# Performance work log

Hardware: AMD Instinct MI355X
Metric: run time of the kernel (lower is better)

## Reference

```python
import jax, jax.numpy as jnp
import numpy as np
import math

N = 512
XDIM = 256
EDIM = 128
N_HEAD = 8
DF = XDIM // N_HEAD


def _linear(x, W, b):
    # torch nn.Linear: y = x @ W.T + b, W is [out, in]
    return x @ W.T + b


def setup_inputs() -> dict:
    key = jax.random.key(0)
    ks = jax.random.split(key, 20)
    s = 0.02
    inp = {
        "x": jax.random.normal(ks[0], (N, XDIM), jnp.float32),
        "e": jax.random.normal(ks[1], (N, N, EDIM), jnp.float32),
        "adj": jax.random.uniform(ks[2], (N, N), jnp.float32),
        "Wq": jax.random.normal(ks[3], (XDIM, XDIM), jnp.float32) * s,
        "bq": jnp.zeros((XDIM,), jnp.float32),
        "Wk": jax.random.normal(ks[4], (XDIM, XDIM), jnp.float32) * s,
        "bk": jnp.zeros((XDIM,), jnp.float32),
        "Wv": jax.random.normal(ks[5], (XDIM, XDIM), jnp.float32) * s,
        "bv": jnp.zeros((XDIM,), jnp.float32),
        "Wem": jax.random.normal(ks[6], (XDIM, EDIM), jnp.float32) * s,
        "bem": jnp.zeros((XDIM,), jnp.float32),
        "Wea": jax.random.normal(ks[7], (XDIM, EDIM), jnp.float32) * s,
        "bea": jnp.zeros((XDIM,), jnp.float32),
        "Wxo": jax.random.normal(ks[8], (XDIM, XDIM), jnp.float32) * s,
        "bxo": jnp.zeros((XDIM,), jnp.float32),
        "Weo": jax.random.normal(ks[9], (EDIM, XDIM), jnp.float32) * s,
        "beo": jnp.zeros((EDIM,), jnp.float32),
    }
    return inp


def reference(x, e, adj, Wq, bq, Wk, bk, Wv, bv, Wem, bem, Wea, bea, Wxo, bxo, Weo, beo):
    n = x.shape[0]
    Q = _linear(x, Wq, bq).reshape(n, N_HEAD, DF)  # [N, H, df]
    K = _linear(x, Wk, bk).reshape(n, N_HEAD, DF)
    # elementwise (non-dot) score: [N, N, H, df]
    Y = (Q[:, None, :, :] * K[None, :, :, :]) / math.sqrt(DF)
    E1 = _linear(e, Wem, bem).reshape(n, n, N_HEAD, DF)
    E2 = _linear(e, Wea, bea).reshape(n, n, N_HEAD, DF)
    Y = Y * (E1 + 1.0) + E2
    newE = _linear(Y.reshape(n, n, XDIM), Weo, beo)  # [N, N, edim]
    attn = jax.nn.softmax(Y, axis=1)  # softmax over key-node axis (dim=1)
    V = _linear(x, Wv, bv).reshape(n, N_HEAD, DF)
    weighted_V = (attn * V[None, :, :, :]).sum(axis=1)  # [N, H, df]
    newX = _linear(weighted_V.reshape(n, XDIM), Wxo, bxo)
    return (newX, newE)
```

## Files before the change

### kernel.cpp

```cpp
#include <hip/hip_runtime.h>
#include <math.h>

#define NN 512
#define XD 256
#define ED 128
#define JC 32
#define NCHUNK (NN/JC)

typedef __attribute__((ext_vector_type(8))) short s8v;
typedef __attribute__((ext_vector_type(4))) float f4v;

__device__ __forceinline__ short f2bf(float f) {
    union { float f; unsigned u; } v; v.f = f;
    unsigned r = (v.u + 0x7FFFu + ((v.u >> 16) & 1u)) >> 16;
    return (short)r;
}
__device__ __forceinline__ s8v load8_bf(const float* __restrict__ p) {
    const float4* p4 = (const float4*)p;
    float4 a = p4[0], b = p4[1];
    s8v r;
    r[0]=f2bf(a.x); r[1]=f2bf(a.y); r[2]=f2bf(a.z); r[3]=f2bf(a.w);
    r[4]=f2bf(b.x); r[5]=f2bf(b.y); r[6]=f2bf(b.z); r[7]=f2bf(b.w);
    return r;
}
__device__ __forceinline__ float bf2f(short s) {
    union { unsigned u; float f; } v;
    v.u = ((unsigned)(unsigned short)s) << 16;
    return v.f;
}

__global__ void wconv_kernel(const float* __restrict__ Wem, const float* __restrict__ Wea,
                             const float* __restrict__ Weo,
                             short* __restrict__ Wem_bf, short* __restrict__ Wea_bf,
                             short* __restrict__ Weo_bf) {
    const int f = blockIdx.x * 256 + threadIdx.x;
    const int lane = f & 63;
    const int quad = lane >> 4;
    const int l16  = lane & 15;
    if (blockIdx.y < 2) {
        const float* src = blockIdx.y == 0 ? Wem : Wea;
        short* dst = blockIdx.y == 0 ? Wem_bf : Wea_bf;
        const int cb = f >> 8;
        const int ks = (f >> 6) & 3;
        *(s8v*)(dst + (size_t)f * 8) =
            load8_bf(src + (size_t)(cb*16 + l16)*ED + ks*32 + quad*8);
    } else {
        const int ob = f >> 9;
        const int ks = (f >> 6) & 7;
        *(s8v*)(Weo_bf + (size_t)f * 8) =
            load8_bf(Weo + (size_t)(ob*16 + l16)*XD + ks*32 + quad*8);
    }
}

__global__ void qkv_kernel(const float* __restrict__ x,
                           const float* __restrict__ Wq, const float* __restrict__ bq,
                           const float* __restrict__ Wk, const float* __restrict__ bk,
                           const float* __restrict__ Wv, const float* __restrict__ bv,
                           float* __restrict__ out) {
    const int i = blockIdx.x, which = blockIdx.y, t = threadIdx.x;
    __shared__ float sx[XD];
    sx[t] = x[i*XD + t];
    __syncthreads();
    const float* W = which==0 ? Wq : (which==1 ? Wk : Wv);
    const float* b = which==0 ? bq : (which==1 ? bk : bv);
    const float4* W4 = (const float4*)(W + (size_t)t*XD);
    const float4* x4 = (const float4*)sx;
    float acc = 0.f;
    #pragma unroll 8
    for (int k4 = 0; k4 < XD/4; ++k4) {
        float4 w = W4[k4]; float4 xv = x4[k4];
        acc += w.x*xv.x + w.y*xv.y + w.z*xv.z + w.w*xv.w;
    }
    acc += b[t];
    if (which == 0) acc *= 0.17677669529663688f;
    out[((size_t)which*NN + i)*XD + t] = acc;
}

#define SE_STRIDE 136
#define SY_STRIDE 264

__global__ __launch_bounds__(512, 4) void pass1_kernel(
    const float* __restrict__ e,
    const float* __restrict__ Qs, const float* __restrict__ Km, const float* __restrict__ Vm,
    const short* __restrict__ Wem_bf, const float* __restrict__ bem,
    const short* __restrict__ Wea_bf, const float* __restrict__ bea,
    const short* __restrict__ Weo_bf, const float* __restrict__ beo,
    float* __restrict__ outE,
    float* __restrict__ Pm, float* __restrict__ Pl, float* __restrict__ Pa)
{
    __shared__ short sE[JC*SE_STRIDE];
    __shared__ short sY[JC*SY_STRIDE];

    const int ch = blockIdx.x;
    const int i  = blockIdx.y;
    const int t = threadIdx.x;
    const int wave = t >> 6;
    const int lane = t & 63;
    const int quad = (lane >> 4) & 3;
    const int l16 = lane & 15;

    const int wn0 = wave * 32;
    float q_l[2], bm1[2], bea_l[2];
    #pragma unroll
    for (int nt = 0; nt < 2; ++nt) {
        const int c = wn0 + nt*16 + l16;
        q_l[nt]   = Qs[i*XD + c];
        bm1[nt]   = bem[c] + 1.0f;
        bea_l[nt] = bea[c];
    }
    const int oo = wave*16 + l16;
    const float beo_l = beo[oo];

    const s8v* W1p = (const s8v*)(Wem_bf + ((size_t)wave*8*64 + lane)*8);
    const s8v* W2p = (const s8v*)(Wea_bf + ((size_t)wave*8*64 + lane)*8);
    const s8v* W3p = (const s8v*)(Weo_bf + ((size_t)wave*8*64 + lane)*8);

    {
        const int j  = t >> 4;
        const int k0 = (t & 15) * 8;
        const float* src = e + ((size_t)i*NN + (size_t)(ch*JC + j))*ED + k0;
        *(s8v*)(&sE[j*SE_STRIDE + k0]) = load8_bf(src);
    }
    __syncthreads();

    f4v acc1[2][2], acc2[2][2];
    #pragma unroll
    for (int mt = 0; mt < 2; ++mt)
        #pragma unroll
        for (int nt = 0; nt < 2; ++nt) {
            f4v z = {0.f, 0.f, 0.f, 0.f};
            acc1[mt][nt] = z; acc2[mt][nt] = z;
        }
    #pragma unroll
    for (int ks = 0; ks < 4; ++ks) {
        s8v a0 = *(const s8v*)(&sE[(     l16)*SE_STRIDE + ks*32 + quad*8]);
        s8v a1 = *(const s8v*)(&sE[(16 + l16)*SE_STRIDE + ks*32 + quad*8]);
        #pragma unroll
        for (int nt = 0; nt < 2; ++nt) {
            s8v b1 = W1p[(nt*4 + ks)*64];
            s8v b2 = W2p[(nt*4 + ks)*64];
            acc1[0][nt] = __builtin_amdgcn_mfma_f32_16x16x32_bf16(a0, b1, acc1[0][nt], 0, 0, 0);
            acc1[1][nt] = __builtin_amdgcn_mfma_f32_16x16x32_bf16(a1, b1, acc1[1][nt], 0, 0, 0);
            acc2[0][nt] = __builtin_amdgcn_mfma_f32_16x16x32_bf16(a0, b2, acc2[0][nt], 0, 0, 0);
            acc2[1][nt] = __builtin_amdgcn_mfma_f32_16x16x32_bf16(a1, b2, acc2[1][nt], 0, 0, 0);
        }
    }

    #pragma unroll
    for (int mt = 0; mt < 2; ++mt) {
        const int jlb = mt*16 + quad*4;
        const int jgb = ch*JC + jlb;
        #pragma unroll
        for (int nt = 0; nt < 2; ++nt) {
            const int c = wn0 + nt*16 + l16;
            #pragma unroll
            for (int r = 0; r < 4; ++r) {
                float e1 = acc1[mt][nt][r] + bm1[nt];
                float e2 = acc2[mt][nt][r] + bea_l[nt];
                float kv = Km[(size_t)(jgb + r)*XD + c];
                float y  = q_l[nt]*kv*e1 + e2;
                sY[(jlb + r)*SY_STRIDE + c] = f2bf(y);
            }
        }
    }
    __syncthreads();

    f4v acc3[2];
    {
        f4v z = {0.f, 0.f, 0.f, 0.f};
        acc3[0] = z; acc3[1] = z;
    }
    #pragma unroll
    for (int ks = 0; ks < 8; ++ks) {
        s8v b3 = W3p[ks*64];
        s8v a0 = *(const s8v*)(&sY[(     l16)*SY_STRIDE + ks*32 + quad*8]);
        s8v a1 = *(const s8v*)(&sY[(16 + l16)*SY_STRIDE + ks*32 + quad*8]);
        acc3[0] = __builtin_amdgcn_mfma_f32_16x16x32_bf16(a0, b3, acc3[0], 0, 0, 0);
        acc3[1] = __builtin_amdgcn_mfma_f32_16x16x32_bf16(a1, b3, acc3[1], 0, 0, 0);
    }
    #pragma unroll
    for (int mt = 0; mt < 2; ++mt) {
        const int jlb = mt*16 + quad*4;
        #pragma unroll
        for (int r = 0; r < 4; ++r) {
            const int jg = ch*JC + jlb + r;
            outE[((size_t)i*NN + jg)*ED + oo] = acc3[mt][r] + beo_l;
        }
    }

    const int sc_c  = t & 255;
    const int sc_jh = t >> 8;
    float m_run = -INFINITY, l_run = 0.f, a_run = 0.f;
    #pragma unroll
    for (int jj = 0; jj < 16; ++jj) {
        const int jl = sc_jh*16 + jj;
        const int jg = ch*JC + jl;
        float y  = bf2f(sY[jl*SY_STRIDE + sc_c]);
        float v  = Vm[(size_t)jg*XD + sc_c];
        float mn = fmaxf(m_run, y);
        float s0 = __expf(m_run - mn);
        float p  = __expf(y - mn);
        l_run = l_run*s0 + p;
        a_run = a_run*s0 + p*v;
        m_run = mn;
    }
    __syncthreads();
    float* sRed = (float*)sE;
    float* sRed2 = (float*)sY;
    sRed[t] = m_run; sRed2[t] = l_run; sRed2[512 + t] = a_run;
    __syncthreads();
    if (t < 256) {
        float m0 = sRed[t],       m1 = sRed[256 + t];
        float l0 = sRed2[t],      l1 = sRed2[256 + t];
        float a0 = sRed2[512+t],  a1 = sRed2[768 + t];
        float M  = fmaxf(m0, m1);
        float e0 = __expf(m0 - M), e1x = __expf(m1 - M);
        const size_t pb = ((size_t)i*NCHUNK + ch)*256 + t;
        Pm[pb] = M;
        Pl[pb] = l0*e0 + l1*e1x;
        Pa[pb] = a0*e0 + a1*e1x;
    }
}

__global__ void pass2_kernel(const float* __restrict__ Pm, const float* __restrict__ Pl,
                             const float* __restrict__ Pa,
                             const float* __restrict__ Wxo, const float* __restrict__ bxo,
                             float* __restrict__ outX) {
    const int i = blockIdx.x, t = threadIdx.x;
    float mloc[NCHUNK];
    float M = -INFINITY;
    #pragma unroll
    for (int ch = 0; ch < NCHUNK; ++ch) {
        mloc[ch] = Pm[((size_t)i*NCHUNK + ch)*256 + t];
        M = fmaxf(M, mloc[ch]);
    }
    float L = 0.f, A = 0.f;
    #pragma unroll
    for (int ch = 0; ch < NCHUNK; ++ch) {
        const size_t pb = ((size_t)i*NCHUNK + ch)*256 + t;
        float s = __expf(mloc[ch] - M);
        L += Pl[pb]*s;
        A += Pa[pb]*s;
    }
    __shared__ float sv[XD];
    sv[t] = A / L;
    __syncthreads();
    const float4* W4 = (const float4*)(Wxo + (size_t)t*XD);
    const float4* v4 = (const float4*)sv;
    float acc = 0.f;
    #pragma unroll 8
    for (int k4 = 0; k4 < XD/4; ++k4) {
        float4 w = W4[k4]; float4 v = v4[k4];
        acc += w.x*v.x + w.y*v.y + w.z*v.z + w.w*v.w;
    }
    outX[(size_t)i*XD + t] = acc + bxo[t];
}

extern "C" void kernel_launch(void* const* d_in, const int* in_sizes, int n_in,
                              void* d_out, int out_size, void* d_ws, size_t ws_size,
                              hipStream_t stream) {
    const float* x   = (const float*)d_in[0];
    const float* e   = (const float*)d_in[1];
    const float* Wq  = (const float*)d_in[3];
    const float* bq  = (const float*)d_in[4];
    const float* Wk  = (const float*)d_in[5];
    const float* bk  = (const float*)d_in[6];
    const float* Wv  = (const float*)d_in[7];
    const float* bv  = (const float*)d_in[8];
    const float* Wem = (const float*)d_in[9];
    const float* bem = (const float*)d_in[10];
    const float* Wea = (const float*)d_in[11];
    const float* bea = (const float*)d_in[12];
    const float* Wxo = (const float*)d_in[13];
    const float* bxo = (const float*)d_in[14];
    const float* Weo = (const float*)d_in[15];
    const float* beo = (const float*)d_in[16];

    float* ws = (float*)d_ws;
    float* Qs = ws;
    float* Km = ws + (size_t)NN*XD;
    float* Vm = ws + (size_t)2*NN*XD;
    float* Pm = ws + (size_t)3*NN*XD;
    float* Pl = Pm + (size_t)NN*NCHUNK*XD;
    float* Pa = Pl + (size_t)NN*NCHUNK*XD;
    short* Wem_bf = (short*)(Pa + (size_t)NN*NCHUNK*XD);
    short* Wea_bf = Wem_bf + (size_t)XD*ED;
    short* Weo_bf = Wea_bf + (size_t)XD*ED;

    float* outX = (float*)d_out;
    float* outE = outX + (size_t)NN*XD;

    wconv_kernel<<<dim3(16, 3), 256, 0, stream>>>(Wem, Wea, Weo, Wem_bf, Wea_bf, Weo_bf);
    qkv_kernel<<<dim3(NN, 3), 256, 0, stream>>>(x, Wq, bq, Wk, bk, Wv, bv, ws);
    pass1_kernel<<<dim3(NCHUNK, NN), 512, 0, stream>>>(e, Qs, Km, Vm,
                                                       Wem_bf, bem, Wea_bf, bea,
                                                       Weo_bf, beo, outE, Pm, Pl, Pa);
    pass2_kernel<<<NN, 256, 0, stream>>>(Pm, Pl, Pa, Wxo, bxo, outX);
}
```

Measured before the change: 389.9 us.

## Fuse pass1 and pass2 into one persistent-per-row kernel with double-buffered e prefetch

```diff
diff --git a/kernel.cpp b/kernel.cpp
--- a/kernel.cpp
+++ b/kernel.cpp
@@ -6,6 +6,8 @@
 #define ED 128
 #define JC 32
 #define NCHUNK (NN/JC)
+#define SE_STRIDE 136
+#define SY_STRIDE 264
 
 typedef __attribute__((ext_vector_type(8))) short s8v;
 typedef __attribute__((ext_vector_type(4))) float f4v;
@@ -23,10 +25,10 @@
     r[4]=f2bf(b.x); r[5]=f2bf(b.y); r[6]=f2bf(b.z); r[7]=f2bf(b.w);
     return r;
 }
-__device__ __forceinline__ float bf2f(short s) {
-    union { unsigned u; float f; } v;
-    v.u = ((unsigned)(unsigned short)s) << 16;
-    return v.f;
+__device__ __forceinline__ unsigned cvt_pk_bf16(float lo, float hi) {
+    unsigned r;
+    asm("v_cvt_pk_bf16_f32 %0, %1, %2" : "=v"(r) : "v"(lo), "v"(hi));
+    return r;
 }
 
 __global__ void wconv_kernel(const float* __restrict__ Wem, const float* __restrict__ Wea,
@@ -76,30 +78,26 @@
     out[((size_t)which*NN + i)*XD + t] = acc;
 }
 
-#define SE_STRIDE 136
-#define SY_STRIDE 264
-
-__global__ __launch_bounds__(512, 4) void pass1_kernel(
+__global__ __launch_bounds__(512, 4) void fused_kernel(
     const float* __restrict__ e,
     const float* __restrict__ Qs, const float* __restrict__ Km, const float* __restrict__ Vm,
     const short* __restrict__ Wem_bf, const float* __restrict__ bem,
     const short* __restrict__ Wea_bf, const float* __restrict__ bea,
     const short* __restrict__ Weo_bf, const float* __restrict__ beo,
-    float* __restrict__ outE,
-    float* __restrict__ Pm, float* __restrict__ Pl, float* __restrict__ Pa)
+    const float* __restrict__ Wxo, const float* __restrict__ bxo,
+    float* __restrict__ outX, float* __restrict__ outE)
 {
-    __shared__ short sE[JC*SE_STRIDE];
-    __shared__ short sY[JC*SY_STRIDE];
-
-    const int ch = blockIdx.x;
-    const int i  = blockIdx.y;
+    __shared__ __align__(16) short sE[2][JC*SE_STRIDE];
+    __shared__ __align__(16) short sY[JC*SY_STRIDE];
+
+    const int i = blockIdx.x;
     const int t = threadIdx.x;
     const int wave = t >> 6;
     const int lane = t & 63;
     const int quad = (lane >> 4) & 3;
-    const int l16 = lane & 15;
-
-    const int wn0 = wave * 32;
+    const int l16  = lane & 15;
+    const int wn0  = wave * 32;
+
     float q_l[2], bm1[2], bea_l[2];
     #pragma unroll
     for (int nt = 0; nt < 2; ++nt) {
@@ -115,145 +113,175 @@
     const s8v* W2p = (const s8v*)(Wea_bf + ((size_t)wave*8*64 + lane)*8);
     const s8v* W3p = (const s8v*)(Weo_bf + ((size_t)wave*8*64 + lane)*8);
 
+    const int sj = t >> 4;
+    const int sk = (t & 15) * 8;
+    const float4* esrc = (const float4*)(e + ((size_t)i*NN + sj)*ED + sk);
+
+    float rm[2] = {-INFINITY, -INFINITY};
+    float rl[2] = {0.f, 0.f};
+    float ra[2] = {0.f, 0.f};
+
+    float4 pfa = esrc[0], pfb = esrc[1];
     {
-        const int j  = t >> 4;
-        const int k0 = (t & 15) * 8;
-        const float* src = e + ((size_t)i*NN + (size_t)(ch*JC + j))*ED + k0;
-        *(s8v*)(&sE[j*SE_STRIDE + k0]) = load8_bf(src);
-    }
+        unsigned u0 = cvt_pk_bf16(pfa.x, pfa.y), u1 = cvt_pk_bf16(pfa.z, pfa.w);
+        unsigned u2 = cvt_pk_bf16(pfb.x, pfb.y), u3 = cvt_pk_bf16(pfb.z, pfb.w);
+        int4 pk; pk.x=(int)u0; pk.y=(int)u1; pk.z=(int)u2; pk.w=(int)u3;
+        *(int4*)(&sE[0][sj*SE_STRIDE + sk]) = pk;
+    }
+    int cur = 0;
+
+    #pragma unroll 1
+    for (int ch = 0; ch < NCHUNK; ++ch) {
+        const bool more = (ch + 1 < NCHUNK);
+        if (more) {
+            const float4* p = esrc + (size_t)(ch+1)*1024;
+            pfa = p[0]; pfb = p[1];
+        }
+        __syncthreads();
+
+        f4v acc1[2][2], acc2[2][2];
+        #pragma unroll
+        for (int mt = 0; mt < 2; ++mt)
+            #pragma unroll
+            for (int nt = 0; nt < 2; ++nt) {
+                f4v z = {0.f, 0.f, 0.f, 0.f};
+                acc1[mt][nt] = z; acc2[mt][nt] = z;
+            }
+        #pragma unroll
+        for (int ks = 0; ks < 4; ++ks) {
+            s8v a0 = *(const s8v*)(&sE[cur][(     l16)*SE_STRIDE + ks*32 + quad*8]);
+            s8v a1 = *(const s8v*)(&sE[cur][(16 + l16)*SE_STRIDE + ks*32 + quad*8]);
+            #pragma unroll
+            for (int nt = 0; nt < 2; ++nt) {
+                s8v b1 = W1p[(nt*4 + ks)*64];
+                s8v b2 = W2p[(nt*4 + ks)*64];
+                acc1[0][nt] = __builtin_amdgcn_mfma_f32_16x16x32_bf16(a0, b1, acc1[0][nt], 0, 0, 0);
+                acc1[1][nt] = __builtin_amdgcn_mfma_f32_16x16x32_bf16(a1, b1, acc1[1][nt], 0, 0, 0);
+                acc2[0][nt] = __builtin_amdgcn_mfma_f32_16x16x32_bf16(a0, b2, acc2[0][nt], 0, 0, 0);
+                acc2[1][nt] = __builtin_amdgcn_mfma_f32_16x16x32_bf16(a1, b2, acc2[1][nt], 0, 0, 0);
+            }
+        }
+
+        float y[2][2][4];
+        const float* Kb = Km + ((size_t)ch*JC + quad*4)*XD + wn0 + l16;
+        #pragma unroll
+        for (int mt = 0; mt < 2; ++mt)
+            #pragma unroll
+            for (int nt = 0; nt < 2; ++nt)
+                #pragma unroll
+                for (int r = 0; r < 4; ++r) {
+                    float e1 = acc1[mt][nt][r] + bm1[nt];
+                    float e2 = acc2[mt][nt][r] + bea_l[nt];
+                    float kv = Kb[(mt*16 + r)*XD + nt*16];
+                    y[mt][nt][r] = q_l[nt]*kv*e1 + e2;
+                }
+
+        #pragma unroll
+        for (int mt = 0; mt < 2; ++mt)
+            #pragma unroll
+            for (int nt = 0; nt < 2; ++nt) {
+                unsigned p01 = cvt_pk_bf16(y[mt][nt][0], y[mt][nt][1]);
+                unsigned p23 = cvt_pk_bf16(y[mt][nt][2], y[mt][nt][3]);
+                short* b = &sY[(mt*16 + quad*4)*SY_STRIDE + wn0 + nt*16 + l16];
+                b[0]            = (short)p01;
+                b[SY_STRIDE]    = (short)(p01 >> 16);
+                b[2*SY_STRIDE]  = (short)p23;
+                b[3*SY_STRIDE]  = (short)(p23 >> 16);
+            }
+
+        {
+            const float* Vb = Vm + ((size_t)ch*JC + quad*4)*XD + wn0 + l16;
+            float vv[2][2][4];
+            #pragma unroll
+            for (int mt = 0; mt < 2; ++mt)
+                #pragma unroll
+                for (int nt = 0; nt < 2; ++nt)
+                    #pragma unroll
+                    for (int r = 0; r < 4; ++r)
+                        vv[mt][nt][r] = Vb[(mt*16 + r)*XD + nt*16];
+            #pragma unroll
+            for (int nt = 0; nt < 2; ++nt) {
+                float mc = fmaxf(
+                    fmaxf(fmaxf(y[0][nt][0], y[0][nt][1]), fmaxf(y[0][nt][2], y[0][nt][3])),
+                    fmaxf(fmaxf(y[1][nt][0], y[1][nt][1]), fmaxf(y[1][nt][2], y[1][nt][3])));
+                float mn = fmaxf(rm[nt], mc);
+                float s  = __expf(rm[nt] - mn);
+                float l0 = rl[nt]*s, a0 = ra[nt]*s;
+                float l1 = 0.f,      a1 = 0.f;
+                #pragma unroll
+                for (int r = 0; r < 4; ++r) {
+                    float p0 = __expf(y[0][nt][r] - mn);
+                    float p1 = __expf(y[1][nt][r] - mn);
+                    l0 += p0; a0 += p0 * vv[0][nt][r];
+                    l1 += p1; a1 += p1 * vv[1][nt][r];
+                }
+                rl[nt] = l0 + l1; ra[nt] = a0 + a1; rm[nt] = mn;
+            }
+        }
+
+        __syncthreads();
+
+        f4v acc3[2];
+        {
+            f4v z = {0.f, 0.f, 0.f, 0.f};
+            acc3[0] = z; acc3[1] = z;
+        }
+        #pragma unroll
+        for (int ks = 0; ks < 8; ++ks) {
+            s8v b3 = W3p[ks*64];
+            s8v a0 = *(const s8v*)(&sY[(     l16)*SY_STRIDE + ks*32 + quad*8]);
+            s8v a1 = *(const s8v*)(&sY[(16 + l16)*SY_STRIDE + ks*32 + quad*8]);
+            acc3[0] = __builtin_amdgcn_mfma_f32_16x16x32_bf16(a0, b3, acc3[0], 0, 0, 0);
+            acc3[1] = __builtin_amdgcn_mfma_f32_16x16x32_bf16(a1, b3, acc3[1], 0, 0, 0);
+        }
+        #pragma unroll
+        for (int mt = 0; mt < 2; ++mt)
+            #pragma unroll
+            for (int r = 0; r < 4; ++r) {
+                const int jg = ch*JC + mt*16 + quad*4 + r;
+                outE[((size_t)i*NN + jg)*ED + oo] = acc3[mt][r] + beo_l;
+            }
+
+        if (more) {
+            unsigned u0 = cvt_pk_bf16(pfa.x, pfa.y), u1 = cvt_pk_bf16(pfa.z, pfa.w);
+            unsigned u2 = cvt_pk_bf16(pfb.x, pfb.y), u3 = cvt_pk_bf16(pfb.z, pfb.w);
+            int4 pk; pk.x=(int)u0; pk.y=(int)u1; pk.z=(int)u2; pk.w=(int)u3;
+            *(int4*)(&sE[cur ^ 1][sj*SE_STRIDE + sk]) = pk;
+            cur ^= 1;
+        }
+    }
+
     __syncthreads();
-
-    f4v acc1[2][2], acc2[2][2];
+    float* sv = (float*)sY;
     #pragma unroll
-    for (int mt = 0; mt < 2; ++mt)
-        #pragma unroll
-        for (int nt = 0; nt < 2; ++nt) {
-            f4v z = {0.f, 0.f, 0.f, 0.f};
-            acc1[mt][nt] = z; acc2[mt][nt] = z;
-        }
-    #pragma unroll
-    for (int ks = 0; ks < 4; ++ks) {
-        s8v a0 = *(const s8v*)(&sE[(     l16)*SE_STRIDE + ks*32 + quad*8]);
-        s8v a1 = *(const s8v*)(&sE[(16 + l16)*SE_STRIDE + ks*32 + quad*8]);
-        #pragma unroll
-        for (int nt = 0; nt < 2; ++nt) {
-            s8v b1 = W1p[(nt*4 + ks)*64];
-            s8v b2 = W2p[(nt*4 + ks)*64];
-            acc1[0][nt] = __builtin_amdgcn_mfma_f32_16x16x32_bf16(a0, b1, acc1[0][nt], 0, 0, 0);
-            acc1[1][nt] = __builtin_amdgcn_mfma_f32_16x16x32_bf16(a1, b1, acc1[1][nt], 0, 0, 0);
-            acc2[0][nt] = __builtin_amdgcn_mfma_f32_16x16x32_bf16(a0, b2, acc2[0][nt], 0, 0, 0);
-            acc2[1][nt] = __builtin_amdgcn_mfma_f32_16x16x32_bf16(a1, b2, acc2[1][nt], 0, 0, 0);
-        }
-    }
-
-    #pragma unroll
-    for (int mt = 0; mt < 2; ++mt) {
-        const int jlb = mt*16 + quad*4;
-        const int jgb = ch*JC + jlb;
-        #pragma unroll
-        for (int nt = 0; nt < 2; ++nt) {
-            const int c = wn0 + nt*16 + l16;
-            #pragma unroll
-            for (int r = 0; r < 4; ++r) {
-                float e1 = acc1[mt][nt][r] + bm1[nt];
-                float e2 = acc2[mt][nt][r] + bea_l[nt];
-                float kv = Km[(size_t)(jgb + r)*XD + c];
-                float y  = q_l[nt]*kv*e1 + e2;
-                sY[(jlb + r)*SY_STRIDE + c] = f2bf(y);
-            }
-        }
+    for (int nt = 0; nt < 2; ++nt) {
+        #pragma unroll
+        for (int off = 16; off < 64; off <<= 1) {
+            float mo = __shfl_xor(rm[nt], off);
+            float lo = __shfl_xor(rl[nt], off);
+            float ao = __shfl_xor(ra[nt], off);
+            float mn = fmaxf(rm[nt], mo);
+            float s  = __expf(rm[nt] - mn);
+            float so = __expf(mo - mn);
+            rl[nt] = rl[nt]*s + lo*so;
+            ra[nt] = ra[nt]*s + ao*so;
+            rm[nt] = mn;
+        }
+        if (quad == 0) sv[wn0 + nt*16 + l16] = ra[nt] / rl[nt];
     }
     __syncthreads();
 
-    f4v acc3[2];
-    {
-        f4v z = {0.f, 0.f, 0.f, 0.f};
-        acc3[0] = z; acc3[1] = z;
-    }
-    #pragma unroll
-    for (int ks = 0; ks < 8; ++ks) {
-        s8v b3 = W3p[ks*64];
-        s8v a0 = *(const s8v*)(&sY[(     l16)*SY_STRIDE + ks*32 + quad*8]);
-        s8v a1 = *(const s8v*)(&sY[(16 + l16)*SY_STRIDE + ks*32 + quad*8]);
-        acc3[0] = __builtin_amdgcn_mfma_f32_16x16x32_bf16(a0, b3, acc3[0], 0, 0, 0);
-        acc3[1] = __builtin_amdgcn_mfma_f32_16x16x32_bf16(a1, b3, acc3[1], 0, 0, 0);
-    }
-    #pragma unroll
-    for (int mt = 0; mt < 2; ++mt) {
-        const int jlb = mt*16 + quad*4;
-        #pragma unroll
-        for (int r = 0; r < 4; ++r) {
-            const int jg = ch*JC + jlb + r;
-            outE[((size_t)i*NN + jg)*ED + oo] = acc3[mt][r] + beo_l;
-        }
-    }
-
-    const int sc_c  = t & 255;
-    const int sc_jh = t >> 8;
-    float m_run = -INFINITY, l_run = 0.f, a_run = 0.f;
-    #pragma unroll
-    for (int jj = 0; jj < 16; ++jj) {
-        const int jl = sc_jh*16 + jj;
-        const int jg = ch*JC + jl;
-        float y  = bf2f(sY[jl*SY_STRIDE + sc_c]);
-        float v  = Vm[(size_t)jg*XD + sc_c];
-        float mn = fmaxf(m_run, y);
-        float s0 = __expf(m_run - mn);
-        float p  = __expf(y - mn);
-        l_run = l_run*s0 + p;
-        a_run = a_run*s0 + p*v;
-        m_run = mn;
-    }
-    __syncthreads();
-    float* sRed = (float*)sE;
-    float* sRed2 = (float*)sY;
-    sRed[t] = m_run; sRed2[t] = l_run; sRed2[512 + t] = a_run;
-    __syncthreads();
-    if (t < 256) {
-        float m0 = sRed[t],       m1 = sRed[256 + t];
-        float l0 = sRed2[t],      l1 = sRed2[256 + t];
-        float a0 = sRed2[512+t],  a1 = sRed2[768 + t];
-        float M  = fmaxf(m0, m1);
-        float e0 = __expf(m0 - M), e1x = __expf(m1 - M);
-        const size_t pb = ((size_t)i*NCHUNK + ch)*256 + t;
-        Pm[pb] = M;
-        Pl[pb] = l0*e0 + l1*e1x;
-        Pa[pb] = a0*e0 + a1*e1x;
-    }
-}
-
-__global__ void pass2_kernel(const float* __restrict__ Pm, const float* __restrict__ Pl,
-                             const float* __restrict__ Pa,
-                             const float* __restrict__ Wxo, const float* __restrict__ bxo,
-                             float* __restrict__ outX) {
-    const int i = blockIdx.x, t = threadIdx.x;
-    float mloc[NCHUNK];
-    float M = -INFINITY;
-    #pragma unroll
-    for (int ch = 0; ch < NCHUNK; ++ch) {
-        mloc[ch] = Pm[((size_t)i*NCHUNK + ch)*256 + t];
-        M = fmaxf(M, mloc[ch]);
-    }
-    float L = 0.f, A = 0.f;
-    #pragma unroll
-    for (int ch = 0; ch < NCHUNK; ++ch) {
-        const size_t pb = ((size_t)i*NCHUNK + ch)*256 + t;
-        float s = __expf(mloc[ch] - M);
-        L += Pl[pb]*s;
-        A += Pa[pb]*s;
-    }
-    __shared__ float sv[XD];
-    sv[t] = A / L;
-    __syncthreads();
-    const float4* W4 = (const float4*)(Wxo + (size_t)t*XD);
-    const float4* v4 = (const float4*)sv;
-    float acc = 0.f;
-    #pragma unroll 8
-    for (int k4 = 0; k4 < XD/4; ++k4) {
-        float4 w = W4[k4]; float4 v = v4[k4];
-        acc += w.x*v.x + w.y*v.y + w.z*v.z + w.w*v.w;
-    }
-    outX[(size_t)i*XD + t] = acc + bxo[t];
+    if (t < XD) {
+        const float4* W4 = (const float4*)(Wxo + (size_t)t*XD);
+        const float4* v4 = (const float4*)sv;
+        float acc = 0.f;
+        #pragma unroll 8
+        for (int k4 = 0; k4 < XD/4; ++k4) {
+            float4 w = W4[k4]; float4 v = v4[k4];
+            acc += w.x*v.x + w.y*v.y + w.z*v.z + w.w*v.w;
+        }
+        outX[(size_t)i*XD + t] = acc + bxo[t];
+    }
 }
 
 extern "C" void kernel_launch(void* const* d_in, const int* in_sizes, int n_in,
@@ -280,10 +308,7 @@
     float* Qs = ws;
     float* Km = ws + (size_t)NN*XD;
     float* Vm = ws + (size_t)2*NN*XD;
-    float* Pm = ws + (size_t)3*NN*XD;
-    float* Pl = Pm + (size_t)NN*NCHUNK*XD;
-    float* Pa = Pl + (size_t)NN*NCHUNK*XD;
-    short* Wem_bf = (short*)(Pa + (size_t)NN*NCHUNK*XD);
+    short* Wem_bf = (short*)(ws + (size_t)3*NN*XD);
     short* Wea_bf = Wem_bf + (size_t)XD*ED;
     short* Weo_bf = Wea_bf + (size_t)XD*ED;
 
@@ -292,8 +317,7 @@
 
     wconv_kernel<<<dim3(16, 3), 256, 0, stream>>>(Wem, Wea, Weo, Wem_bf, Wea_bf, Weo_bf);
     qkv_kernel<<<dim3(NN, 3), 256, 0, stream>>>(x, Wq, bq, Wk, bk, Wv, bv, ws);
-    pass1_kernel<<<dim3(NCHUNK, NN), 512, 0, stream>>>(e, Qs, Km, Vm,
-                                                       Wem_bf, bem, Wea_bf, bea,
-                                                       Weo_bf, beo, outE, Pm, Pl, Pa);
-    pass2_kernel<<<NN, 256, 0, stream>>>(Pm, Pl, Pa, Wxo, bxo, outX);
-}
+    fused_kernel<<<NN, 512, 0, stream>>>(e, Qs, Km, Vm,
+                                         Wem_bf, bem, Wea_bf, bea, Weo_bf, beo,
+                                         Wxo, bxo, outX, outE);
+}
```

Measured after the change: 482.8 us. 1.24x slower.

## Compute chunk softmax partials from MFMA registers with wave shuffles

Applied to the files above, without the earlier changes.

```diff
diff --git a/kernel.cpp b/kernel.cpp
--- a/kernel.cpp
+++ b/kernel.cpp
@@ -6,6 +6,8 @@
 #define ED 128
 #define JC 32
 #define NCHUNK (NN/JC)
+#define SE_STRIDE 136
+#define SY_STRIDE 264
 
 typedef __attribute__((ext_vector_type(8))) short s8v;
 typedef __attribute__((ext_vector_type(4))) float f4v;
@@ -23,10 +25,10 @@
     r[4]=f2bf(b.x); r[5]=f2bf(b.y); r[6]=f2bf(b.z); r[7]=f2bf(b.w);
     return r;
 }
-__device__ __forceinline__ float bf2f(short s) {
-    union { unsigned u; float f; } v;
-    v.u = ((unsigned)(unsigned short)s) << 16;
-    return v.f;
+__device__ __forceinline__ unsigned cvt_pk_bf16(float lo, float hi) {
+    unsigned r;
+    asm("v_cvt_pk_bf16_f32 %0, %1, %2" : "=v"(r) : "v"(lo), "v"(hi));
+    return r;
 }
 
 __global__ void wconv_kernel(const float* __restrict__ Wem, const float* __restrict__ Wea,
@@ -76,9 +78,6 @@
     out[((size_t)which*NN + i)*XD + t] = acc;
 }
 
-#define SE_STRIDE 136
-#define SY_STRIDE 264
-
 __global__ __launch_bounds__(512, 4) void pass1_kernel(
     const float* __restrict__ e,
     const float* __restrict__ Qs, const float* __restrict__ Km, const float* __restrict__ Vm,
@@ -88,8 +87,8 @@
     float* __restrict__ outE,
     float* __restrict__ Pm, float* __restrict__ Pl, float* __restrict__ Pa)
 {
-    __shared__ short sE[JC*SE_STRIDE];
-    __shared__ short sY[JC*SY_STRIDE];
+    __shared__ __align__(16) short sE[JC*SE_STRIDE];
+    __shared__ __align__(16) short sY[JC*SY_STRIDE];
 
     const int ch = blockIdx.x;
     const int i  = blockIdx.y;
@@ -98,8 +97,8 @@
     const int lane = t & 63;
     const int quad = (lane >> 4) & 3;
     const int l16 = lane & 15;
-
     const int wn0 = wave * 32;
+
     float q_l[2], bm1[2], bea_l[2];
     #pragma unroll
     for (int nt = 0; nt < 2; ++nt) {
@@ -116,11 +115,27 @@
     const s8v* W3p = (const s8v*)(Weo_bf + ((size_t)wave*8*64 + lane)*8);
 
     {
-        const int j  = t >> 4;
-        const int k0 = (t & 15) * 8;
-        const float* src = e + ((size_t)i*NN + (size_t)(ch*JC + j))*ED + k0;
-        *(s8v*)(&sE[j*SE_STRIDE + k0]) = load8_bf(src);
-    }
+        const int sj = t >> 4;
+        const int sk = (t & 15) * 8;
+        const float4* p4 = (const float4*)(e + ((size_t)i*NN + (size_t)(ch*JC + sj))*ED + sk);
+        float4 a = p4[0], b = p4[1];
+        unsigned u0 = cvt_pk_bf16(a.x, a.y), u1 = cvt_pk_bf16(a.z, a.w);
+        unsigned u2 = cvt_pk_bf16(b.x, b.y), u3 = cvt_pk_bf16(b.z, b.w);
+        int4 pk; pk.x=(int)u0; pk.y=(int)u1; pk.z=(int)u2; pk.w=(int)u3;
+        *(int4*)(&sE[sj*SE_STRIDE + sk]) = pk;
+    }
+
+    const float* Kb = Km + ((size_t)(ch*JC) + quad*4)*XD + wn0 + l16;
+    const float* Vb = Vm + ((size_t)(ch*JC) + quad*4)*XD + wn0 + l16;
+    float kv[2][2][4];
+    #pragma unroll
+    for (int mt = 0; mt < 2; ++mt)
+        #pragma unroll
+        for (int nt = 0; nt < 2; ++nt)
+            #pragma unroll
+            for (int r = 0; r < 4; ++r)
+                kv[mt][nt][r] = Kb[(mt*16 + r)*XD + nt*16];
+
     __syncthreads();
 
     f4v acc1[2][2], acc2[2][2];
@@ -146,23 +161,63 @@
         }
     }
 
-    #pragma unroll
-    for (int mt = 0; mt < 2; ++mt) {
-        const int jlb = mt*16 + quad*4;
-        const int jgb = ch*JC + jlb;
-        #pragma unroll
-        for (int nt = 0; nt < 2; ++nt) {
-            const int c = wn0 + nt*16 + l16;
+    float y[2][2][4];
+    #pragma unroll
+    for (int mt = 0; mt < 2; ++mt)
+        #pragma unroll
+        for (int nt = 0; nt < 2; ++nt)
             #pragma unroll
             for (int r = 0; r < 4; ++r) {
                 float e1 = acc1[mt][nt][r] + bm1[nt];
                 float e2 = acc2[mt][nt][r] + bea_l[nt];
-                float kv = Km[(size_t)(jgb + r)*XD + c];
-                float y  = q_l[nt]*kv*e1 + e2;
-                sY[(jlb + r)*SY_STRIDE + c] = f2bf(y);
+                y[mt][nt][r] = q_l[nt]*kv[mt][nt][r]*e1 + e2;
             }
-        }
-    }
+
+    #pragma unroll
+    for (int mt = 0; mt < 2; ++mt)
+        #pragma unroll
+        for (int nt = 0; nt < 2; ++nt) {
+            unsigned p01 = cvt_pk_bf16(y[mt][nt][0], y[mt][nt][1]);
+            unsigned p23 = cvt_pk_bf16(y[mt][nt][2], y[mt][nt][3]);
+            short* b = &sY[(mt*16 + quad*4)*SY_STRIDE + wn0 + nt*16 + l16];
+            b[0]            = (short)p01;
+            b[SY_STRIDE]    = (short)(p01 >> 16);
+            b[2*SY_STRIDE]  = (short)p23;
+            b[3*SY_STRIDE]  = (short)(p23 >> 16);
+        }
+
+    float Mc[2], Lc[2], Ac[2];
+    {
+        float vv[2][2][4];
+        #pragma unroll
+        for (int mt = 0; mt < 2; ++mt)
+            #pragma unroll
+            for (int nt = 0; nt < 2; ++nt)
+                #pragma unroll
+                for (int r = 0; r < 4; ++r)
+                    vv[mt][nt][r] = Vb[(mt*16 + r)*XD + nt*16];
+        #pragma unroll
+        for (int nt = 0; nt < 2; ++nt) {
+            float m = fmaxf(
+                fmaxf(fmaxf(y[0][nt][0], y[0][nt][1]), fmaxf(y[0][nt][2], y[0][nt][3])),
+                fmaxf(fmaxf(y[1][nt][0], y[1][nt][1]), fmaxf(y[1][nt][2], y[1][nt][3])));
+            m = fmaxf(m, __shfl_xor(m, 16));
+            m = fmaxf(m, __shfl_xor(m, 32));
+            float l = 0.f, a = 0.f;
+            #pragma unroll
+            for (int mt = 0; mt < 2; ++mt)
+                #pragma unroll
+                for (int r = 0; r < 4; ++r) {
+                    float p = __expf(y[mt][nt][r] - m);
+                    l += p;
+                    a += p * vv[mt][nt][r];
+                }
+            l += __shfl_xor(l, 16); l += __shfl_xor(l, 32);
+            a += __shfl_xor(a, 16); a += __shfl_xor(a, 32);
+            Mc[nt] = m; Lc[nt] = l; Ac[nt] = a;
+        }
+    }
+
     __syncthreads();
 
     f4v acc3[2];
@@ -179,46 +234,21 @@
         acc3[1] = __builtin_amdgcn_mfma_f32_16x16x32_bf16(a1, b3, acc3[1], 0, 0, 0);
     }
     #pragma unroll
-    for (int mt = 0; mt < 2; ++mt) {
-        const int jlb = mt*16 + quad*4;
+    for (int mt = 0; mt < 2; ++mt)
         #pragma unroll
         for (int r = 0; r < 4; ++r) {
-            const int jg = ch*JC + jlb + r;
+            const int jg = ch*JC + mt*16 + quad*4 + r;
             outE[((size_t)i*NN + jg)*ED + oo] = acc3[mt][r] + beo_l;
         }
-    }
-
-    const int sc_c  = t & 255;
-    const int sc_jh = t >> 8;
-    float m_run = -INFINITY, l_run = 0.f, a_run = 0.f;
-    #pragma unroll
-    for (int jj = 0; jj < 16; ++jj) {
-        const int jl = sc_jh*16 + jj;
-        const int jg = ch*JC + jl;
-        float y  = bf2f(sY[jl*SY_STRIDE + sc_c]);
-        float v  = Vm[(size_t)jg*XD + sc_c];
-        float mn = fmaxf(m_run, y);
-        float s0 = __expf(m_run - mn);
-        float p  = __expf(y - mn);
-        l_run = l_run*s0 + p;
-        a_run = a_run*s0 + p*v;
-        m_run = mn;
-    }
-    __syncthreads();
-    float* sRed = (float*)sE;
-    float* sRed2 = (float*)sY;
-    sRed[t] = m_run; sRed2[t] = l_run; sRed2[512 + t] = a_run;
-    __syncthreads();
-    if (t < 256) {
-        float m0 = sRed[t],       m1 = sRed[256 + t];
-        float l0 = sRed2[t],      l1 = sRed2[256 + t];
-        float a0 = sRed2[512+t],  a1 = sRed2[768 + t];
-        float M  = fmaxf(m0, m1);
-        float e0 = __expf(m0 - M), e1x = __expf(m1 - M);
-        const size_t pb = ((size_t)i*NCHUNK + ch)*256 + t;
-        Pm[pb] = M;
-        Pl[pb] = l0*e0 + l1*e1x;
-        Pa[pb] = a0*e0 + a1*e1x;
+
+    if (quad == 0) {
+        #pragma unroll
+        for (int nt = 0; nt < 2; ++nt) {
+            const size_t pb = ((size_t)i*NCHUNK + ch)*256 + wn0 + nt*16 + l16;
+            Pm[pb] = Mc[nt];
+            Pl[pb] = Lc[nt];
+            Pa[pb] = Ac[nt];
+        }
     }
 }
 
```

Result: no change. 384.8 us (-1.3%).
